# Performance work log

Hardware: AMD Instinct MI355X
Metric: run time of the kernel (lower is better)

Reference implementation:

```python
import jax, jax.numpy as jnp
import numpy as np

NY, NU, NHIDDEN = 64, 64, 256
NHRZ, NBATCH = 1024, 128


def setup_inputs() -> dict:
    key = jax.random.key(0)
    ks = jax.random.split(key, 9)
    y0 = jax.random.normal(ks[0], (NBATCH, NY), dtype=jnp.float32)
    U = jax.random.normal(ks[1], (NHRZ, NBATCH, NU), dtype=jnp.float32)
    # parameters (match torch init: uniform(0,1) for continuous eigen params,
    # randn/sqrt(Nu) for B, Kaiming-uniform-ish for Linear layers)
    lmbd_cont_real = jax.random.uniform(ks[2], (NHIDDEN // 2,), dtype=jnp.float32)
    lmbd_cont_imag = jax.random.uniform(ks[3], (NHIDDEN // 2,), dtype=jnp.float32)
    B = jax.random.normal(ks[4], (NHIDDEN, NU), dtype=jnp.float32) / np.sqrt(NU)
    lim1 = 1.0 / np.sqrt(NY)
    W_y2x = jax.random.uniform(ks[5], (NHIDDEN, NY), dtype=jnp.float32, minval=-lim1, maxval=lim1)
    b_y2x = jax.random.uniform(ks[6], (NHIDDEN,), dtype=jnp.float32, minval=-lim1, maxval=lim1)
    lim2 = 1.0 / np.sqrt(NHIDDEN)
    W_x2y = jax.random.uniform(ks[7], (NY, NHIDDEN), dtype=jnp.float32, minval=-lim2, maxval=lim2)
    b_x2y = jax.random.uniform(ks[8], (NY,), dtype=jnp.float32, minval=-lim2, maxval=lim2)
    return {"y0": y0, "U": U, "lmbd_cont_real": lmbd_cont_real,
            "lmbd_cont_imag": lmbd_cont_imag, "B": B,
            "W_y2x": W_y2x, "b_y2x": b_y2x, "W_x2y": W_x2y, "b_x2y": b_x2y}


def reference(y0, U, lmbd_cont_real, lmbd_cont_imag, B, W_y2x, b_y2x, W_x2y, b_x2y):
    n = lmbd_cont_real.shape[0]  # Nhidden // 2
    r = jnp.exp(-jnp.abs(lmbd_cont_real))
    theta = (np.pi / 2.0) * lmbd_cont_imag
    lmbd_real = r * jnp.cos(theta)  # [n]
    lmbd_imag = r * jnp.sin(theta)  # [n]
    nf = jnp.sqrt(1.0 - jnp.exp(-2.0 * jnp.abs(lmbd_cont_real)))
    nf = jnp.concatenate([nf, nf])  # [Nhidden]
    # Bu[t,b,h] = (U @ B^T) * nf
    Bu = jnp.einsum('tbu,hu->tbh', U, B) * nf  # [Nhrz, Nbatch, Nhidden]
    x0 = y0 @ W_y2x.T + b_y2x  # [Nbatch, Nhidden]

    # x @ A^T with A = [[diag(lr), -diag(li)], [diag(li), diag(lr)]] is a
    # per-pair 2x2 rotation -> pure elementwise ops (same math, no dense matmul)
    def step(x, bu):
        x1, x2 = x[:, :n], x[:, n:]
        xn = jnp.concatenate([lmbd_real * x1 - lmbd_imag * x2,
                              lmbd_imag * x1 + lmbd_real * x2], axis=-1) + bu
        return xn, xn

    _, X = jax.lax.scan(step, x0, Bu)  # X: [Nhrz, Nbatch, Nhidden]
    Y = X @ W_x2y.T + b_x2y  # [Nhrz, Nbatch, Ny]
    return Y
```

## Files before the change

### kernel.cpp

```cpp
#include <hip/hip_runtime.h>
#include <stdint.h>

#define T_HRZ 1024
#define NBAT  128
#define NHID  256
#define NPAIR 128
#define NUIN  64
#define NYOUT 64
#define LCH   16
#define CCH   64

#define WS_LAM   0
#define WS_LAML  256
#define WS_LPOW  512
#define WS_X0P   4608
#define WS_WBU   37376
#define WS_WBY   45568
#define WS_S     53760
#define WS_E     2150912
#define WS_P     4248064

typedef __attribute__((ext_vector_type(8))) short short8;
typedef __attribute__((ext_vector_type(4))) float float4v;

__device__ __forceinline__ unsigned int f2bf_bits(float x) {
  unsigned int u = __float_as_uint(x);
  return (u + 0x7fffu + ((u >> 16) & 1u)) >> 16;
}

__global__ __launch_bounds__(256) void k_prep(
    const float* __restrict__ y0, const float* __restrict__ lrc,
    const float* __restrict__ lic, const float* __restrict__ Bm,
    const float* __restrict__ Wy2x, const float* __restrict__ by2x,
    const float* __restrict__ Wx2y, float* __restrict__ ws)
{
  int blk = blockIdx.x;
  int h = threadIdx.x;
  if (blk < NBAT) {
    __shared__ float y0s[NYOUT];
    if (h < NYOUT) y0s[h] = y0[blk * NYOUT + h];
    __syncthreads();
    float acc = by2x[h];
    const float* wr = Wy2x + h * NYOUT;
#pragma unroll 16
    for (int k = 0; k < NYOUT; ++k) acc += y0s[k] * wr[k];
    int j = h & (NPAIR - 1);
    int comp = h >> 7;
    ws[WS_X0P + (blk * NPAIR + j) * 2 + comp] = acc;
  } else if (blk == NBAT) {
    if (h < NPAIR) {
      float a  = fabsf(lrc[h]);
      float r  = expf(-a);
      float th = 1.5707963267948966f * lic[h];
      float lr = r * cosf(th);
      float li = r * sinf(th);
      ws[WS_LAM + h]         = lr;
      ws[WS_LAM + NPAIR + h] = li;
      float2* lp = (float2*)(ws + WS_LPOW);
      float pr = lr, pi_ = li;
      lp[0 * NPAIR + h] = make_float2(pr, pi_);
      for (int l = 1; l < LCH; ++l) {
        float nr = pr * lr - pi_ * li;
        float ni = pr * li + pi_ * lr;
        pr = nr; pi_ = ni;
        lp[l * NPAIR + h] = make_float2(pr, pi_);
      }
      ws[WS_LAML + h]         = pr;
      ws[WS_LAML + NPAIR + h] = pi_;
    }
  } else if (blk == NBAT + 1) {
    unsigned short* wbu = (unsigned short*)(ws + WS_WBU);
    for (int idx = h; idx < 16384; idx += 256) {
      int nt   = idx >> 10;
      int kk   = (idx >> 9) & 1;
      int lane = (idx >> 3) & 63;
      int jj   = idx & 7;
      int u  = kk * 32 + (lane >> 4) * 8 + jj;
      int hh = nt * 16 + (lane & 15);
      float a2 = fabsf(lrc[hh & (NPAIR - 1)]);
      float nf = sqrtf(1.f - expf(-2.f * a2));
      wbu[idx] = (unsigned short)f2bf_bits(Bm[hh * NUIN + u] * nf);
    }
  } else {
    unsigned short* wby = (unsigned short*)(ws + WS_WBY);
    for (int idx = h; idx < 16384; idx += 256) {
      int nt   = idx >> 12;
      int kk   = (idx >> 9) & 7;
      int lane = (idx >> 3) & 63;
      int jj   = idx & 7;
      int hh = kk * 32 + (lane >> 4) * 8 + jj;
      int y  = nt * 16 + (lane & 15);
      wby[idx] = (unsigned short)f2bf_bits(Wx2y[y * NHID + hh]);
    }
  }
}

__global__ __launch_bounds__(128) void k_phaseA(
    const float* __restrict__ U, float* __restrict__ ws)
{
  int c = blockIdx.x, b = blockIdx.y;
  int tid = threadIdx.x, wave = tid >> 6, lane = tid & 63;
  int m = lane & 15, quad = lane >> 4;
  __shared__ float X32[LCH * 260];

  const float* urow = U + ((size_t)(c * LCH + m) * NBAT + b) * NUIN;
  short8 afr[2];
#pragma unroll
  for (int kk = 0; kk < 2; ++kk) {
    int u0 = kk * 32 + quad * 8;
    float4 va = *(const float4*)(urow + u0);
    float4 vb = *(const float4*)(urow + u0 + 4);
    short8 f;
    f[0] = (short)f2bf_bits(va.x); f[1] = (short)f2bf_bits(va.y);
    f[2] = (short)f2bf_bits(va.z); f[3] = (short)f2bf_bits(va.w);
    f[4] = (short)f2bf_bits(vb.x); f[5] = (short)f2bf_bits(vb.y);
    f[6] = (short)f2bf_bits(vb.z); f[7] = (short)f2bf_bits(vb.w);
    afr[kk] = f;
  }

  const short8* wbu = (const short8*)(ws + WS_WBU);
  float4v z = {0.f, 0.f, 0.f, 0.f};
  float4v acc[8];
#pragma unroll
  for (int n = 0; n < 8; ++n) acc[n] = z;
#pragma unroll
  for (int n = 0; n < 8; ++n) {
    int nt = wave * 8 + n;
    acc[n] = __builtin_amdgcn_mfma_f32_16x16x32_bf16(afr[0], wbu[(nt * 2 + 0) * 64 + lane], acc[n], 0, 0, 0);
    acc[n] = __builtin_amdgcn_mfma_f32_16x16x32_bf16(afr[1], wbu[(nt * 2 + 1) * 64 + lane], acc[n], 0, 0, 0);
  }

#pragma unroll
  for (int n = 0; n < 8; ++n) {
    int hh = (wave * 8 + n) * 16 + (lane & 15);
#pragma unroll
    for (int r = 0; r < 4; ++r)
      X32[(quad * 4 + r) * 260 + hh] = acc[n][r];
  }
  __syncthreads();

  int j = tid;
  float lr = ws[WS_LAM + j], li = ws[WS_LAM + NPAIR + j];
  float s1 = 0.f, s2 = 0.f;
  unsigned int* P = (unsigned int*)(ws + WS_P);
#pragma unroll
  for (int l = 0; l < LCH; ++l) {
    float v1 = X32[l * 260 + j];
    float v2 = X32[l * 260 + NPAIR + j];
    float n1 = lr * s1 - li * s2 + v1;
    float n2 = li * s1 + lr * s2 + v2;
    s1 = n1; s2 = n2;
    P[((size_t)(c * LCH + l) * NBAT + b) * NPAIR + j] =
        f2bf_bits(s1) | (f2bf_bits(s2) << 16);
  }
  ((float2*)(ws + WS_S))[((size_t)c * NBAT + b) * NPAIR + j] = make_float2(s1, s2);
}

__global__ __launch_bounds__(128) void k_phaseB(float* __restrict__ ws)
{
  int b = blockIdx.x, j = threadIdx.x;
  float e1 = ws[WS_X0P + (b * NPAIR + j) * 2 + 0];
  float e2 = ws[WS_X0P + (b * NPAIR + j) * 2 + 1];
  float Lr = ws[WS_LAML + j], Li = ws[WS_LAML + NPAIR + j];
  const float2* sp = (const float2*)(ws + WS_S);
  float2* ep = (float2*)(ws + WS_E);
  const size_t cs = (size_t)NBAT * NPAIR;
  size_t o0 = (size_t)b * NPAIR + j;
  float2 buf[8];
#pragma unroll
  for (int k = 0; k < 8; ++k) buf[k] = sp[k * cs + o0];
  for (int g = 0; g < 8; ++g) {
    float2 nxt[8];
    if (g < 7) {
#pragma unroll
      for (int k = 0; k < 8; ++k) nxt[k] = sp[(size_t)((g + 1) * 8 + k) * cs + o0];
    }
#pragma unroll
    for (int k = 0; k < 8; ++k) {
      ep[(size_t)(g * 8 + k) * cs + o0] = make_float2(e1, e2);
      float n1 = Lr * e1 - Li * e2 + buf[k].x;
      float n2 = Li * e1 + Lr * e2 + buf[k].y;
      e1 = n1; e2 = n2;
    }
    if (g < 7) {
#pragma unroll
      for (int k = 0; k < 8; ++k) buf[k] = nxt[k];
    }
  }
}

__global__ __launch_bounds__(128) void k_phaseC(
    const float* __restrict__ bx2y, float* __restrict__ out,
    float* __restrict__ ws)
{
  int c = blockIdx.x, b = blockIdx.y;
  int tid = threadIdx.x, wave = tid >> 6, lane = tid & 63;
  __shared__ unsigned short XA[8 * 64 * 8];

  int j = tid;
  float2 e = ((const float2*)(ws + WS_E))[((size_t)c * NBAT + b) * NPAIR + j];
  const float2* lp = (const float2*)(ws + WS_LPOW);
  const unsigned int* P = (const unsigned int*)(ws + WS_P);
  int h1 = j, h2 = j + NPAIR;
  int base1 = ((h1 >> 5) << 9) + (((h1 >> 3) & 3) << 7) + (h1 & 7);
  int base2 = ((h2 >> 5) << 9) + (((h2 >> 3) & 3) << 7) + (h2 & 7);
#pragma unroll
  for (int l = 0; l < LCH; ++l) {
    float2 lpv = lp[l * NPAIR + j];
    unsigned int pk = P[((size_t)(c * LCH + l) * NBAT + b) * NPAIR + j];
    float b1 = __uint_as_float(pk << 16);
    float b2 = __uint_as_float(pk & 0xffff0000u);
    float x1 = lpv.x * e.x - lpv.y * e.y + b1;
    float x2 = lpv.y * e.x + lpv.x * e.y + b2;
    XA[base1 + l * 8] = (unsigned short)f2bf_bits(x1);
    XA[base2 + l * 8] = (unsigned short)f2bf_bits(x2);
  }
  __syncthreads();

  const short8* xa = (const short8*)XA;
  const short8* wby = (const short8*)(ws + WS_WBY);
  float4v z = {0.f, 0.f, 0.f, 0.f};
  float4v acc0 = z, acc1 = z;
  int nt0 = wave * 2, nt1 = nt0 + 1;
#pragma unroll
  for (int kk = 0; kk < 8; ++kk) {
    short8 a = xa[kk * 64 + lane];
    acc0 = __builtin_amdgcn_mfma_f32_16x16x32_bf16(a, wby[(nt0 * 8 + kk) * 64 + lane], acc0, 0, 0, 0);
    acc1 = __builtin_amdgcn_mfma_f32_16x16x32_bf16(a, wby[(nt1 * 8 + kk) * 64 + lane], acc1, 0, 0, 0);
  }

  int col = lane & 15, quad = lane >> 4;
  float bias0 = bx2y[nt0 * 16 + col];
  float bias1 = bx2y[nt1 * 16 + col];
#pragma unroll
  for (int r = 0; r < 4; ++r) {
    int row = quad * 4 + r;
    size_t o = ((size_t)(c * LCH + row) * NBAT + b) * NYOUT;
    out[o + nt0 * 16 + col] = acc0[r] + bias0;
    out[o + nt1 * 16 + col] = acc1[r] + bias1;
  }
}

extern "C" void kernel_launch(void* const* d_in, const int* in_sizes, int n_in,
                              void* d_out, int out_size, void* d_ws, size_t ws_size,
                              hipStream_t stream) {
  (void)in_sizes; (void)n_in; (void)out_size; (void)ws_size;
  const float* y0   = (const float*)d_in[0];
  const float* U    = (const float*)d_in[1];
  const float* lrc  = (const float*)d_in[2];
  const float* lic  = (const float*)d_in[3];
  const float* Bm   = (const float*)d_in[4];
  const float* Wy2x = (const float*)d_in[5];
  const float* by2x = (const float*)d_in[6];
  const float* Wx2y = (const float*)d_in[7];
  const float* bx2y = (const float*)d_in[8];
  float* out = (float*)d_out;
  float* ws  = (float*)d_ws;

  k_prep<<<dim3(NBAT + 3), 256, 0, stream>>>(y0, lrc, lic, Bm, Wy2x, by2x, Wx2y, ws);
  k_phaseA<<<dim3(CCH, NBAT), 128, 0, stream>>>(U, ws);
  k_phaseB<<<dim3(NBAT), 128, 0, stream>>>(ws);
  k_phaseC<<<dim3(CCH, NBAT), 128, 0, stream>>>(bx2y, out, ws);
}
```

Before: 164.7 us.

## Recompute local chunk scan in phase C instead of storing partial states

Phase A no longer writes per-step bf16 local scan states to workspace. Phase C instead reloads U, recomputes Bu with MFMA and reruns the 16-step recurrence starting from the chunk's carried-in state. This removes a large intermediate write and read in exchange for reading U a second time and duplicating the input-projection matmul. The precomputed lambda-power table is also dropped, and phase C uses more shared memory.

```diff
diff --git a/kernel.cpp b/kernel.cpp
--- a/kernel.cpp
+++ b/kernel.cpp
@@ -12,13 +12,11 @@
 
 #define WS_LAM   0
 #define WS_LAML  256
-#define WS_LPOW  512
-#define WS_X0P   4608
-#define WS_WBU   37376
-#define WS_WBY   45568
-#define WS_S     53760
-#define WS_E     2150912
-#define WS_P     4248064
+#define WS_X0P   512
+#define WS_WBU   33280
+#define WS_WBY   41472
+#define WS_S     49664
+#define WS_E     2146816
 
 typedef __attribute__((ext_vector_type(8))) short short8;
 typedef __attribute__((ext_vector_type(4))) float float4v;
@@ -56,14 +54,11 @@
       float li = r * sinf(th);
       ws[WS_LAM + h]         = lr;
       ws[WS_LAM + NPAIR + h] = li;
-      float2* lp = (float2*)(ws + WS_LPOW);
       float pr = lr, pi_ = li;
-      lp[0 * NPAIR + h] = make_float2(pr, pi_);
       for (int l = 1; l < LCH; ++l) {
         float nr = pr * lr - pi_ * li;
         float ni = pr * li + pi_ * lr;
         pr = nr; pi_ = ni;
-        lp[l * NPAIR + h] = make_float2(pr, pi_);
       }
       ws[WS_LAML + h]         = pr;
       ws[WS_LAML + NPAIR + h] = pi_;
@@ -142,7 +137,6 @@
   int j = tid;
   float lr = ws[WS_LAM + j], li = ws[WS_LAM + NPAIR + j];
   float s1 = 0.f, s2 = 0.f;
-  unsigned int* P = (unsigned int*)(ws + WS_P);
 #pragma unroll
   for (int l = 0; l < LCH; ++l) {
     float v1 = X32[l * 260 + j];
@@ -150,8 +144,6 @@
     float n1 = lr * s1 - li * s2 + v1;
     float n2 = li * s1 + lr * s2 + v2;
     s1 = n1; s2 = n2;
-    P[((size_t)(c * LCH + l) * NBAT + b) * NPAIR + j] =
-        f2bf_bits(s1) | (f2bf_bits(s2) << 16);
   }
   ((float2*)(ws + WS_S))[((size_t)c * NBAT + b) * NPAIR + j] = make_float2(s1, s2);
 }
@@ -190,28 +182,66 @@
 }
 
 __global__ __launch_bounds__(128) void k_phaseC(
-    const float* __restrict__ bx2y, float* __restrict__ out,
-    float* __restrict__ ws)
+    const float* __restrict__ U, const float* __restrict__ bx2y,
+    float* __restrict__ out, float* __restrict__ ws)
 {
   int c = blockIdx.x, b = blockIdx.y;
   int tid = threadIdx.x, wave = tid >> 6, lane = tid & 63;
+  int m = lane & 15, quad = lane >> 4;
+  __shared__ float X32[LCH * 260];
   __shared__ unsigned short XA[8 * 64 * 8];
 
+  const float* urow = U + ((size_t)(c * LCH + m) * NBAT + b) * NUIN;
+  short8 afr[2];
+#pragma unroll
+  for (int kk = 0; kk < 2; ++kk) {
+    int u0 = kk * 32 + quad * 8;
+    float4 va = *(const float4*)(urow + u0);
+    float4 vb = *(const float4*)(urow + u0 + 4);
+    short8 f;
+    f[0] = (short)f2bf_bits(va.x); f[1] = (short)f2bf_bits(va.y);
+    f[2] = (short)f2bf_bits(va.z); f[3] = (short)f2bf_bits(va.w);
+    f[4] = (short)f2bf_bits(vb.x); f[5] = (short)f2bf_bits(vb.y);
+    f[6] = (short)f2bf_bits(vb.z); f[7] = (short)f2bf_bits(vb.w);
+    afr[kk] = f;
+  }
+
+  const short8* wbu = (const short8*)(ws + WS_WBU);
+  float4v z = {0.f, 0.f, 0.f, 0.f};
+  {
+    float4v acc[8];
+#pragma unroll
+    for (int n = 0; n < 8; ++n) acc[n] = z;
+#pragma unroll
+    for (int n = 0; n < 8; ++n) {
+      int nt = wave * 8 + n;
+      acc[n] = __builtin_amdgcn_mfma_f32_16x16x32_bf16(afr[0], wbu[(nt * 2 + 0) * 64 + lane], acc[n], 0, 0, 0);
+      acc[n] = __builtin_amdgcn_mfma_f32_16x16x32_bf16(afr[1], wbu[(nt * 2 + 1) * 64 + lane], acc[n], 0, 0, 0);
+    }
+#pragma unroll
+    for (int n = 0; n < 8; ++n) {
+      int hh = (wave * 8 + n) * 16 + (lane & 15);
+#pragma unroll
+      for (int r = 0; r < 4; ++r)
+        X32[(quad * 4 + r) * 260 + hh] = acc[n][r];
+    }
+  }
+  __syncthreads();
+
   int j = tid;
+  float lr = ws[WS_LAM + j], li = ws[WS_LAM + NPAIR + j];
   float2 e = ((const float2*)(ws + WS_E))[((size_t)c * NBAT + b) * NPAIR + j];
-  const float2* lp = (const float2*)(ws + WS_LPOW);
-  const unsigned int* P = (const unsigned int*)(ws + WS_P);
+  float x1 = e.x, x2 = e.y;
   int h1 = j, h2 = j + NPAIR;
   int base1 = ((h1 >> 5) << 9) + (((h1 >> 3) & 3) << 7) + (h1 & 7);
   int base2 = ((h2 >> 5) << 9) + (((h2 >> 3) & 3) << 7) + (h2 & 7);
 #pragma unroll
   for (int l = 0; l < LCH; ++l) {
-    float2 lpv = lp[l * NPAIR + j];
-    unsigned int pk = P[((size_t)(c * LCH + l) * NBAT + b) * NPAIR + j];
-    float b1 = __uint_as_float(pk << 16);
-    float b2 = __uint_as_float(pk & 0xffff0000u);
-    float x1 = lpv.x * e.x - lpv.y * e.y + b1;
-    float x2 = lpv.y * e.x + lpv.x * e.y + b2;
+    float v1 = X32[l * 260 + j];
+    float v2 = X32[l * 260 + NPAIR + j];
+    float n1 = lr * x1 - li * x2 + v1;
+    float n2 = li * x1 + lr * x2 + v2;
+    x1 = n1; x2 = n2;
     XA[base1 + l * 8] = (unsigned short)f2bf_bits(x1);
     XA[base2 + l * 8] = (unsigned short)f2bf_bits(x2);
   }
@@ -219,7 +249,6 @@
 
   const short8* xa = (const short8*)XA;
   const short8* wby = (const short8*)(ws + WS_WBY);
-  float4v z = {0.f, 0.f, 0.f, 0.f};
   float4v acc0 = z, acc1 = z;
   int nt0 = wave * 2, nt1 = nt0 + 1;
 #pragma unroll
@@ -229,7 +258,7 @@
     acc1 = __builtin_amdgcn_mfma_f32_16x16x32_bf16(a, wby[(nt1 * 8 + kk) * 64 + lane], acc1, 0, 0, 0);
   }
 
-  int col = lane & 15, quad = lane >> 4;
+  int col = lane & 15;
   float bias0 = bx2y[nt0 * 16 + col];
   float bias1 = bx2y[nt1 * 16 + col];
 #pragma unroll
@@ -260,5 +289,5 @@
   k_prep<<<dim3(NBAT + 3), 256, 0, stream>>>(y0, lrc, lic, Bm, Wy2x, by2x, Wx2y, ws);
   k_phaseA<<<dim3(CCH, NBAT), 128, 0, stream>>>(U, ws);
   k_phaseB<<<dim3(NBAT), 128, 0, stream>>>(ws);
-  k_phaseC<<<dim3(CCH, NBAT), 128, 0, stream>>>(bx2y, out, ws);
-}
+  k_phaseC<<<dim3(CCH, NBAT), 128, 0, stream>>>(U, bx2y, out, ws);
+}
```

Result: no change. 167.7 us (+1.8%).
